# Kernel optimization log

Measured on AMD Instinct MI355X. Metric: run time of the kernel, lower is better.

Reference implementation:

```python
import jax, jax.numpy as jnp
import numpy as np

N = 1048576  # param.N, number of memory slots
W = 64       # param.W, word width
R = 4        # number of read heads
EPS = 1e-8   # torch cosine_similarity eps


def setup_inputs() -> dict:
    key = jax.random.key(0)
    ks = jax.random.split(key, 7)
    return {
        "desired_content": jax.random.normal(ks[0], (W,), dtype=jnp.float32),
        "memory": jax.random.normal(ks[1], (N, W), dtype=jnp.float32),
        "key_strength": jax.random.uniform(ks[2], (1,), dtype=jnp.float32) + 1.0,  # beta in [1, inf)
        "free_gate": jax.random.uniform(ks[3], (R,), dtype=jnp.float32),
        "read_weighting": jax.random.uniform(ks[4], (N, R), dtype=jnp.float32),
        "previous_usage": jax.random.uniform(ks[5], (N,), dtype=jnp.float32),
        "write_weighting": jax.random.uniform(ks[6], (N,), dtype=jnp.float32),
    }


def reference(desired_content, memory, key_strength, free_gate,
              read_weighting, previous_usage, write_weighting):
    # ---- content_lookup: cosine similarity of key vs every memory row, softmax over N
    key_norm = jnp.maximum(jnp.linalg.norm(desired_content), EPS)
    row_norms = jnp.maximum(jnp.linalg.norm(memory, axis=1), EPS)  # (N,)
    sim = (memory @ desired_content) / (row_norms * key_norm)       # (N,)
    content_weighting = jax.nn.softmax(sim * key_strength[0])       # (N,)

    # ---- memory_retention: prod over read heads of (1 - w_r * f_r)
    retention = jnp.prod(1.0 - read_weighting * free_gate[None, :], axis=1)  # (N,)

    # ---- usage_vector
    usage = (previous_usage + write_weighting - previous_usage * write_weighting) * retention  # (N,)

    # ---- allocation_weighting (faithful to the original loop, including its use of
    # (1 - sorted[i]) for slot indices[i+1]):
    #   ret[idx[0]] = 1 - s[0]
    #   ret[idx[j]] = (1 - s[j-1]) * prod_{i<j} s[i]   for j >= 1
    idx = jnp.argsort(usage)                     # ascending usage order
    s = usage[idx]                               # sorted usages, (N,)
    shifted = jnp.concatenate([s[:1], s[:-1]])   # s[max(j-1,0)]
    excl_cumprod = jnp.concatenate([jnp.ones((1,), s.dtype), jnp.cumprod(s[:-1])])
    alloc_sorted = (1.0 - shifted) * excl_cumprod
    allocation = jnp.zeros_like(usage).at[idx].set(alloc_sorted)  # scatter back to natural order

    return jnp.stack([content_weighting, retention, usage, allocation])  # (4, N)
```

## Files before the change

kernel.cpp:

```cpp
#include <hip/hip_runtime.h>
#include <math.h>

#define NSL   1048576u
#define WW    64
#define NBLK  4096
#define CAP   131072
#define SORTN 2048
#define NBINS 2048
#define UTH   0.005f

#define WS_PART 4
#define WS_CVAL 8192
#define WS_CIDX (8192 + CAP)

__global__ __launch_bounds__(256) void k_main(
    const float* __restrict__ mem, const float* __restrict__ key,
    const float* __restrict__ beta, const float* __restrict__ fg,
    const float* __restrict__ rw,  const float* __restrict__ pu,
    const float* __restrict__ wwt,
    float* __restrict__ out, float* __restrict__ ws)
{
    __shared__ float kbuf[WW];
    __shared__ float c_sh;
    __shared__ float part[4];
    int tid = threadIdx.x;
    if (tid < WW / 4) ((float4*)kbuf)[tid] = ((const float4*)key)[tid];
    __syncthreads();
    if (tid < 64) {
        float x = kbuf[tid];
        float s = x * x;
        #pragma unroll
        for (int off = 32; off > 0; off >>= 1) s += __shfl_down(s, off);
        if (tid == 0) c_sh = beta[0] / fmaxf(sqrtf(s), 1e-8f);
    }
    __syncthreads();

    int w = tid >> 6;
    int L = tid & 63;
    unsigned int R0 = blockIdx.x * 256u + (unsigned int)(w * 64);
    float4 kf = ((const float4*)kbuf)[L & 15];

    const float4* mbase = (const float4*)mem + (size_t)R0 * (WW / 4);

    float myDot = 0.f, myNr = 0.f;
    #pragma unroll
    for (int j = 0; j < 16; ++j) {
        float4 m = mbase[j * 64 + L];
        float d = m.x * kf.x + m.y * kf.y + m.z * kf.z + m.w * kf.w;
        float q = m.x * m.x + m.y * m.y + m.z * m.z + m.w * m.w;
        #pragma unroll
        for (int msk = 1; msk < 16; msk <<= 1) {
            d += __shfl_xor(d, msk, 64);
            q += __shfl_xor(q, msk, 64);
        }
        float dg = __shfl(d, (L & 3) << 4, 64);
        float qg = __shfl(q, (L & 3) << 4, 64);
        if ((L >> 2) == j) { myDot = dg; myNr = qg; }
    }

    unsigned int n = R0 + (unsigned int)L;
    float rn = fmaxf(sqrtf(myNr), 1e-8f);
    float e = __expf(c_sh * myDot / rn);
    out[n] = e;

    float4 r = ((const float4*)rw)[n];
    float4 g = *((const float4*)fg);
    float ret = (1.f - r.x * g.x) * (1.f - r.y * g.y) *
                (1.f - r.z * g.z) * (1.f - r.w * g.w);
    float p = pu[n], w2 = wwt[n];
    float u = (p + w2 - p * w2) * ret;

    out[NSL + n]      = ret;
    out[2u * NSL + n] = u;
    out[3u * NSL + n] = 0.f;

    if (u < UTH) {
        unsigned int pos = atomicAdd((unsigned int*)ws + 2, 1u);
        if (pos < CAP) {
            ws[WS_CVAL + pos] = u;
            ((unsigned int*)ws)[WS_CIDX + pos] = n;
        }
    }

    float s = e;
    #pragma unroll
    for (int off = 32; off > 0; off >>= 1) s += __shfl_down(s, off);
    if ((tid & 63) == 0) part[tid >> 6] = s;
    __syncthreads();
    if (tid == 0) ws[WS_PART + blockIdx.x] = part[0] + part[1] + part[2] + part[3];
}

__global__ __launch_bounds__(512) void k_select(float* __restrict__ out,
                                                float* __restrict__ ws)
{
    __shared__ unsigned long long sk[SORTN];
    __shared__ unsigned int hist[NBINS];
    __shared__ unsigned int csum[512];
    __shared__ float pr[8];
    __shared__ unsigned long long wr2[8];
    __shared__ unsigned long long last_sh;
    __shared__ unsigned int c2_sh;
    __shared__ int bcut_sh;
    int tid = threadIdx.x;

    float s = 0.f;
    for (int i = tid; i < NBLK; i += 512) s += ws[WS_PART + i];
    #pragma unroll
    for (int off = 32; off > 0; off >>= 1) s += __shfl_down(s, off);
    if ((tid & 63) == 0) pr[tid >> 6] = s;
    __syncthreads();
    if (tid == 0) {
        float t = 0.f;
        #pragma unroll
        for (int i = 0; i < 8; ++i) t += pr[i];
        ws[1] = 1.f / t;
    }

    int M = (int)((const unsigned int*)ws)[2];
    if (M > CAP) M = CAP;

    int Msort = -1;

    if (M <= SORTN) {
        for (int i = tid; i < SORTN; i += 512) {
            unsigned long long kk = ~0ull;
            if (i < M)
                kk = ((unsigned long long)__float_as_uint(ws[WS_CVAL + i]) << 32)
                     | (unsigned long long)((const unsigned int*)ws)[WS_CIDX + i];
            sk[i] = kk;
        }
        Msort = M;
        __syncthreads();
    } else {
        for (int i = tid; i < NBINS; i += 512) hist[i] = 0u;
        __syncthreads();
        for (int i = tid; i < M; i += 512) {
            unsigned int b = __float_as_uint(ws[WS_CVAL + i]) >> 19;
            atomicAdd(&hist[b], 1u);
        }
        __syncthreads();
        {
            unsigned int s4 = 0;
            #pragma unroll
            for (int k = 0; k < 4; ++k) s4 += hist[tid * 4 + k];
            csum[tid] = s4;
        }
        __syncthreads();
        if (tid == 0) {
            unsigned int acc = 0;
            int B = NBINS - 1;
            for (int c = 0; c < 512; ++c) {
                if (acc + csum[c] >= 64u) {
                    unsigned int a2 = acc;
                    for (int k = 0; k < 4; ++k) {
                        a2 += hist[c * 4 + k];
                        if (a2 >= 64u) { B = c * 4 + k; break; }
                    }
                    break;
                }
                acc += csum[c];
            }
            bcut_sh = B;
            c2_sh = 0u;
        }
        __syncthreads();
        unsigned int B = (unsigned int)bcut_sh;
        for (int i = tid; i < SORTN; i += 512) sk[i] = ~0ull;
        __syncthreads();
        for (int i = tid; i < M; i += 512) {
            float v = ws[WS_CVAL + i];
            if ((__float_as_uint(v) >> 19) <= B) {
                unsigned int p = atomicAdd(&c2_sh, 1u);
                if (p < SORTN)
                    sk[p] = ((unsigned long long)__float_as_uint(v) << 32)
                            | (unsigned long long)((const unsigned int*)ws)[WS_CIDX + i];
            }
        }
        __syncthreads();
        unsigned int C2 = c2_sh;
        if (C2 <= SORTN) Msort = (int)C2;
    }

    if (Msort >= 0) {
        for (int k2 = 2; k2 <= SORTN; k2 <<= 1) {
            for (int j = k2 >> 1; j > 0; j >>= 1) {
                for (int i = tid; i < SORTN; i += 512) {
                    int ixj = i ^ j;
                    if (ixj > i) {
                        bool up = ((i & k2) == 0);
                        unsigned long long a = sk[i], b = sk[ixj];
                        if (up ? (a > b) : (a < b)) { sk[i] = b; sk[ixj] = a; }
                    }
                }
                __syncthreads();
            }
        }
        if (tid == 0) {
            float cum = 1.f, prev = 0.f;
            int K = Msort < 64 ? Msort : 64;
            for (int k = 0; k < K; ++k) {
                unsigned long long b = sk[k];
                float v = __uint_as_float((unsigned int)(b >> 32));
                unsigned int slot = (unsigned int)b;
                float a = (1.f - (k == 0 ? v : prev)) * cum;
                out[3u * NSL + slot] = a;
                cum *= v; prev = v;
            }
        }
    } else {
        if (tid == 0) last_sh = 0ull;
        __syncthreads();
        float cum = 1.f, prev = 0.f;
        int K = M < 64 ? M : 64;
        for (int k = 0; k < K; ++k) {
            unsigned long long last = last_sh;
            unsigned long long best = ~0ull;
            for (int i = tid; i < M; i += 512) {
                unsigned long long kk =
                    ((unsigned long long)__float_as_uint(ws[WS_CVAL + i]) << 32)
                    | (unsigned long long)((const unsigned int*)ws)[WS_CIDX + i];
                if ((k == 0 || kk > last) && kk < best) best = kk;
            }
            #pragma unroll
            for (int off = 32; off > 0; off >>= 1) {
                unsigned long long o = __shfl_down(best, off);
                if (o < best) best = o;
            }
            if ((tid & 63) == 0) wr2[tid >> 6] = best;
            __syncthreads();
            if (tid == 0) {
                unsigned long long b = ~0ull;
                #pragma unroll
                for (int i = 0; i < 8; ++i) if (wr2[i] < b) b = wr2[i];
                float v = __uint_as_float((unsigned int)(b >> 32));
                unsigned int slot = (unsigned int)b;
                float a = (1.f - (k == 0 ? v : prev)) * cum;
                out[3u * NSL + slot] = a;
                cum *= v; prev = v;
                last_sh = b;
            }
            __syncthreads();
        }
    }
}

__global__ __launch_bounds__(256) void k_norm(float* __restrict__ out,
                                              const float* __restrict__ ws) {
    unsigned int i = blockIdx.x * 256u + threadIdx.x;
    float inv = ws[1];
    float4* o = (float4*)out;
    float4 v = o[i];
    v.x *= inv; v.y *= inv; v.z *= inv; v.w *= inv;
    o[i] = v;
}

extern "C" void kernel_launch(void* const* d_in, const int* in_sizes, int n_in,
                              void* d_out, int out_size, void* d_ws, size_t ws_size,
                              hipStream_t stream) {
    const float* key  = (const float*)d_in[0];
    const float* mem  = (const float*)d_in[1];
    const float* beta = (const float*)d_in[2];
    const float* fg   = (const float*)d_in[3];
    const float* rw   = (const float*)d_in[4];
    const float* pu   = (const float*)d_in[5];
    const float* wwt  = (const float*)d_in[6];
    float* out = (float*)d_out;
    float* ws  = (float*)d_ws;

    hipMemsetAsync(ws, 0, 32, stream);
    k_main<<<dim3(NBLK), dim3(256), 0, stream>>>(mem, key, beta, fg, rw, pu, wwt, out, ws);
    k_select<<<dim3(1), dim3(512), 0, stream>>>(out, ws);
    k_norm<<<dim3(NSL / 4 / 256), dim3(256), 0, stream>>>(out, ws);
}
```

Measured before the change: 441.7 us.

## Restructure row dot-product mapping, hoist side loads, and size bitonic sort to candidates

Each row's 64 floats are now read by 4 lanes holding 16 floats each, instead of 16 lanes holding 4 floats each. This replaces the 4-step xor shuffle tree run 16 times with a 2-step tree run 4 times, cutting cross-lane traffic. The per-slot read_weighting, usage and write loads are issued before the memory loop so their latency overlaps it. The bitonic sort now covers only the next power of two at or above the candidate count (minimum 64) rather than a fixed 2048, which relies on the padded entries being max-keyed sentinels.

```diff
diff --git a/kernel.cpp b/kernel.cpp
--- a/kernel.cpp
+++ b/kernel.cpp
@@ -38,36 +38,48 @@
     int w = tid >> 6;
     int L = tid & 63;
     unsigned int R0 = blockIdx.x * 256u + (unsigned int)(w * 64);
-    float4 kf = ((const float4*)kbuf)[L & 15];
-
-    const float4* mbase = (const float4*)mem + (size_t)R0 * (WW / 4);
+    unsigned int n = R0 + (unsigned int)L;
+
+    float4 r  = ((const float4*)rw)[n];
+    float4 g  = *((const float4*)fg);
+    float  p  = pu[n], w2 = wwt[n];
+
+    int c = L & 3;
+    float4 kf0 = ((const float4*)kbuf)[c * 4 + 0];
+    float4 kf1 = ((const float4*)kbuf)[c * 4 + 1];
+    float4 kf2 = ((const float4*)kbuf)[c * 4 + 2];
+    float4 kf3 = ((const float4*)kbuf)[c * 4 + 3];
+
+    const float4* mbase = (const float4*)mem
+                        + (size_t)R0 * (WW / 4)
+                        + (size_t)(L >> 2) * (WW / 4) + (size_t)c * 4;
 
     float myDot = 0.f, myNr = 0.f;
     #pragma unroll
-    for (int j = 0; j < 16; ++j) {
-        float4 m = mbase[j * 64 + L];
-        float d = m.x * kf.x + m.y * kf.y + m.z * kf.z + m.w * kf.w;
-        float q = m.x * m.x + m.y * m.y + m.z * m.z + m.w * m.w;
-        #pragma unroll
-        for (int msk = 1; msk < 16; msk <<= 1) {
-            d += __shfl_xor(d, msk, 64);
-            q += __shfl_xor(q, msk, 64);
-        }
-        float dg = __shfl(d, (L & 3) << 4, 64);
-        float qg = __shfl(q, (L & 3) << 4, 64);
-        if ((L >> 2) == j) { myDot = dg; myNr = qg; }
-    }
-
-    unsigned int n = R0 + (unsigned int)L;
+    for (int j = 0; j < 4; ++j) {
+        const float4* pj = mbase + j * 16 * (WW / 4);
+        float4 m0 = pj[0], m1 = pj[1], m2 = pj[2], m3 = pj[3];
+        float d = m0.x * kf0.x + m0.y * kf0.y + m0.z * kf0.z + m0.w * kf0.w
+                + m1.x * kf1.x + m1.y * kf1.y + m1.z * kf1.z + m1.w * kf1.w
+                + m2.x * kf2.x + m2.y * kf2.y + m2.z * kf2.z + m2.w * kf2.w
+                + m3.x * kf3.x + m3.y * kf3.y + m3.z * kf3.z + m3.w * kf3.w;
+        float q = m0.x * m0.x + m0.y * m0.y + m0.z * m0.z + m0.w * m0.w
+                + m1.x * m1.x + m1.y * m1.y + m1.z * m1.z + m1.w * m1.w
+                + m2.x * m2.x + m2.y * m2.y + m2.z * m2.z + m2.w * m2.w
+                + m3.x * m3.x + m3.y * m3.y + m3.z * m3.z + m3.w * m3.w;
+        d += __shfl_xor(d, 1, 64); d += __shfl_xor(d, 2, 64);
+        q += __shfl_xor(q, 1, 64); q += __shfl_xor(q, 2, 64);
+        float dg = __shfl(d, (L & 15) << 2, 64);
+        float qg = __shfl(q, (L & 15) << 2, 64);
+        if ((L >> 4) == j) { myDot = dg; myNr = qg; }
+    }
+
     float rn = fmaxf(sqrtf(myNr), 1e-8f);
     float e = __expf(c_sh * myDot / rn);
     out[n] = e;
 
-    float4 r = ((const float4*)rw)[n];
-    float4 g = *((const float4*)fg);
     float ret = (1.f - r.x * g.x) * (1.f - r.y * g.y) *
                 (1.f - r.z * g.z) * (1.f - r.w * g.w);
-    float p = pu[n], w2 = wwt[n];
     float u = (p + w2 - p * w2) * ret;
 
     out[NSL + n]      = ret;
@@ -182,9 +194,11 @@
     }
 
     if (Msort >= 0) {
-        for (int k2 = 2; k2 <= SORTN; k2 <<= 1) {
+        int SN = 64;
+        while (SN < Msort) SN <<= 1;
+        for (int k2 = 2; k2 <= SN; k2 <<= 1) {
             for (int j = k2 >> 1; j > 0; j >>= 1) {
-                for (int i = tid; i < SORTN; i += 512) {
+                for (int i = tid; i < SN; i += 512) {
                     int ixj = i ^ j;
                     if (ixj > i) {
                         bool up = ((i & k2) == 0);
```

Result: no change. 439.4 us (-0.5%).
